# Performance work log

Measured on AMD Instinct MI355X. Metric: run time of the kernel, lower is better.

Reference implementation:

```python
import jax, jax.numpy as jnp
import numpy as np

SHAPES = ((80, 80), (40, 40), (20, 20), (10, 10))  # (H, W) per level
N_HEADS = 8
N_POINTS = 4
D_MODEL = 512  # double_d_model = 2*256 (densefusion=True)
D_FFN = 1024
B = 2
L = len(SHAPES)
S = sum(h * w for h, w in SHAPES)  # 8500
EPS = 1e-5


def _layernorm(x, g, b):
    m = jnp.mean(x, axis=-1, keepdims=True)
    v = jnp.mean((x - m) ** 2, axis=-1, keepdims=True)
    return (x - m) * jax.lax.rsqrt(v + EPS) * g + b


def _reference_points(shapes):
    # encoder get_reference_points with valid_ratios == 1 -> [S, 2] (x, y) in (0,1)
    refs = []
    for (H, W) in shapes:
        ry = (jnp.arange(H, dtype=jnp.float32) + 0.5) / H
        rx = (jnp.arange(W, dtype=jnp.float32) + 0.5) / W
        gy, gx = jnp.meshgrid(ry, rx, indexing='ij')
        refs.append(jnp.stack([gx.reshape(-1), gy.reshape(-1)], axis=-1))
    return jnp.concatenate(refs, axis=0)


def _sample_level(val, loc, H, W):
    # val: [B, H*W, h, d]; loc: [B, S, h, P, 2] normalized in [0,1]
    b, _, h, d = val.shape
    s, p = loc.shape[1], loc.shape[3]
    x = loc[..., 0] * W - 0.5
    y = loc[..., 1] * H - 0.5
    x0 = jnp.floor(x)
    y0 = jnp.floor(y)
    wx = x - x0
    wy = y - y0
    x0i = x0.astype(jnp.int32)
    y0i = y0.astype(jnp.int32)

    def gather(xi, yi):
        valid = ((xi >= 0) & (xi < W) & (yi >= 0) & (yi < H)).astype(val.dtype)
        idx = jnp.clip(yi, 0, H - 1) * W + jnp.clip(xi, 0, W - 1)  # [B,S,h,P]
        idx2 = jnp.transpose(idx, (0, 1, 3, 2)).reshape(b, s * p, h)  # [B,S*P,h]
        g = jnp.take_along_axis(val, idx2[..., None], axis=1)  # [B,S*P,h,d]
        vmask = jnp.transpose(valid, (0, 1, 3, 2))[..., None]  # [B,S,P,h,1]
        return g.reshape(b, s, p, h, d) * vmask

    v00 = gather(x0i, y0i)
    v01 = gather(x0i + 1, y0i)
    v10 = gather(x0i, y0i + 1)
    v11 = gather(x0i + 1, y0i + 1)
    wxT = jnp.transpose(wx, (0, 1, 3, 2))[..., None]
    wyT = jnp.transpose(wy, (0, 1, 3, 2))[..., None]
    return (v00 * (1 - wxT) * (1 - wyT) + v01 * wxT * (1 - wyT)
            + v10 * (1 - wxT) * wyT + v11 * wxT * wyT)  # [B,S,P,h,d]


def _forward(src, pos, w_off, b_off, w_attn, b_attn, w_val, b_val, w_out, b_out,
             ln1_g, ln1_b, w1, b1, w2, b2, ln2_g, ln2_b, shapes):
    b, s, c = src.shape
    h, p, l = N_HEADS, N_POINTS, len(shapes)
    d = c // h
    q = src + pos
    value = (src @ w_val + b_val).reshape(b, s, h, d)
    offsets = (q @ w_off + b_off).reshape(b, s, h, l, p, 2)
    attn = jax.nn.softmax((q @ w_attn + b_attn).reshape(b, s, h, l * p), axis=-1)
    attn = attn.reshape(b, s, h, l, p)
    ref = _reference_points(shapes)  # [S,2]
    # offset normalizer = (W_l, H_l)
    norm = jnp.array([[W, H] for (H, W) in shapes], dtype=src.dtype)  # [L,2]
    loc = ref[None, :, None, None, None, :] + offsets / norm[None, None, None, :, None, :]
    # split value per level and sample
    starts = np.cumsum([0] + [H * W for (H, W) in shapes])[:-1]
    sampled = []
    for lvl, (H, W) in enumerate(shapes):
        val_l = jax.lax.dynamic_slice_in_dim(value, int(starts[lvl]), H * W, axis=1)
        sampled.append(_sample_level(val_l, loc[:, :, :, lvl], H, W))
    sampled = jnp.stack(sampled)  # [L,B,S,P,h,d]
    out = jnp.einsum('lbqphd,bqhlp->bqhd', sampled, attn).reshape(b, s, c)
    attn_out = out @ w_out + b_out
    x = _layernorm(src + attn_out, ln1_g, ln1_b)
    ffn = jax.nn.relu(x @ w1 + b1) @ w2 + b2
    return _layernorm(x + ffn, ln2_g, ln2_b)


def setup_inputs() -> dict:
    key = jax.random.key(0)
    ks = jax.random.split(key, 20)
    sc = 0.02
    C = D_MODEL
    hLP = N_HEADS * L * N_POINTS
    f32 = jnp.float32
    inp = {
        'src': jax.random.normal(ks[0], (B, S, C), f32),
        'pos': jax.random.normal(ks[1], (B, S, C), f32),
        'w_off': jax.random.normal(ks[2], (C, hLP * 2), f32) * sc,
        'b_off': jax.random.normal(ks[3], (hLP * 2,), f32) * sc,
        'w_attn': jax.random.normal(ks[4], (C, hLP), f32) * sc,
        'b_attn': jax.random.normal(ks[5], (hLP,), f32) * sc,
        'w_val': jax.random.normal(ks[6], (C, C), f32) * sc,
        'b_val': jnp.zeros((C,), f32),
        'w_out': jax.random.normal(ks[7], (C, C), f32) * sc,
        'b_out': jnp.zeros((C,), f32),
        'ln1_g': jnp.ones((C,), f32),
        'ln1_b': jnp.zeros((C,), f32),
        'w1': jax.random.normal(ks[8], (C, D_FFN), f32) * sc,
        'b1': jnp.zeros((D_FFN,), f32),
        'w2': jax.random.normal(ks[9], (D_FFN, C), f32) * sc,
        'b2': jnp.zeros((C,), f32),
        'ln2_g': jnp.ones((C,), f32),
        'ln2_b': jnp.zeros((C,), f32),
        'spatial_shapes': jnp.array(SHAPES, dtype=jnp.int32),
    }
    return inp


def reference(src, pos, w_off, b_off, w_attn, b_attn, w_val, b_val, w_out, b_out,
              ln1_g, ln1_b, w1, b1, w2, b2, ln2_g, ln2_b, spatial_shapes):
    shapes = tuple((int(a), int(b)) for a, b in np.asarray(spatial_shapes))
    return _forward(src, pos, w_off, b_off, w_attn, b_attn, w_val, b_val, w_out, b_out,
                    ln1_g, ln1_b, w1, b1, w2, b2, ln2_g, ln2_b, shapes)
```

## Files before the change

### kernel.cpp

```cpp
#include <hip/hip_runtime.h>


typedef __bf16 bf16_t;
typedef __bf16 bf16x8 __attribute__((ext_vector_type(8)));
typedef __bf16 bf16x4 __attribute__((ext_vector_type(4)));
typedef float  f32x4  __attribute__((ext_vector_type(4)));
typedef float  f32x16 __attribute__((ext_vector_type(16)));

#define M_ROWS 17000
#define S_LEN  8500

__device__ inline void store_c(float* p, float v)  { *p = v; }
__device__ inline void store_c(bf16_t* p, float v) { *p = (bf16_t)v; }

__device__ inline float4 load4f(const float* p)  { return *(const float4*)p; }
__device__ inline float4 load4f(const bf16_t* p) {
    bf16x4 v = *(const bf16x4*)p;
    return make_float4((float)v[0], (float)v[1], (float)v[2], (float)v[3]);
}

__global__ __launch_bounds__(256)
void prep_kernel(const float* __restrict__ w_val, const float* __restrict__ w_off,
                 const float* __restrict__ w_attn, const float* __restrict__ w_out,
                 const float* __restrict__ w1, const float* __restrict__ w2,
                 const float* __restrict__ b_off, const float* __restrict__ b_attn,
                 bf16_t* __restrict__ wt_val, bf16_t* __restrict__ wt_oa,
                 bf16_t* __restrict__ wt_out, bf16_t* __restrict__ wt_w1,
                 bf16_t* __restrict__ wt_w2, float* __restrict__ bias_oa) {
    int z = blockIdx.z;
    if (z == 6) {
        if (blockIdx.x == 0 && blockIdx.y == 0) {
            for (int i = threadIdx.x; i < 384; i += 256)
                bias_oa[i] = (i < 256) ? b_off[i] : b_attn[i - 256];
        }
        return;
    }
    const float* in; bf16_t* out; int K, N;
    switch (z) {
        case 0: in = w_val;  out = wt_val;                     K = 512;  N = 512;  break;
        case 1: in = w_off;  out = wt_oa;                      K = 512;  N = 256;  break;
        case 2: in = w_attn; out = wt_oa + (size_t)256 * 512;  K = 512;  N = 128;  break;
        case 3: in = w_out;  out = wt_out;                     K = 512;  N = 512;  break;
        case 4: in = w1;     out = wt_w1;                      K = 512;  N = 1024; break;
        default: in = w2;    out = wt_w2;                      K = 1024; N = 512;  break;
    }
    int k0 = blockIdx.x * 32, n0 = blockIdx.y * 32;
    if (k0 >= K || n0 >= N) return;
    __shared__ float s[32][33];
    int tx = threadIdx.x & 31, ty = threadIdx.x >> 5;
    #pragma unroll
    for (int i = 0; i < 4; i++)
        s[ty + 8 * i][tx] = in[(size_t)(k0 + ty + 8 * i) * N + n0 + tx];
    __syncthreads();
    #pragma unroll
    for (int i = 0; i < 4; i++)
        out[(size_t)(n0 + ty + 8 * i) * K + k0 + tx] = (bf16_t)s[tx][ty + 8 * i];
}

__global__ __launch_bounds__(256)
void add_q_kernel(const float* __restrict__ a, const float* __restrict__ b,
                  bf16_t* __restrict__ q, bf16_t* __restrict__ src_bf, int n4) {
    int i = blockIdx.x * 256 + threadIdx.x;
    if (i >= n4) return;
    float4 av = *(const float4*)(a + (size_t)i * 4);
    float4 bv = *(const float4*)(b + (size_t)i * 4);
    bf16x4 sv, ov;
    sv[0] = (bf16_t)av.x; sv[1] = (bf16_t)av.y; sv[2] = (bf16_t)av.z; sv[3] = (bf16_t)av.w;
    ov[0] = (bf16_t)(av.x + bv.x);
    ov[1] = (bf16_t)(av.y + bv.y);
    ov[2] = (bf16_t)(av.z + bv.z);
    ov[3] = (bf16_t)(av.w + bv.w);
    *(bf16x4*)(q      + (size_t)i * 4) = ov;
    *(bf16x4*)(src_bf + (size_t)i * 4) = sv;
}

#define GEMM_CORE(A_PTR, WT_PTR, K_DIM, EPILOGUE)                                  \
    const int tid  = threadIdx.x;                                                  \
    const int wave = tid >> 6;                                                     \
    const int lane = tid & 63;                                                     \
    const int l31  = lane & 31;                                                    \
    const int lh8  = (lane >> 5) * 8;                                              \
    const int wr   = (wave >> 1) * 64;                                             \
    const int wc   = (wave & 1) * 64;                                              \
    const int row0 = blockIdx.x * 128;                                             \
    const int sr = tid >> 2;                                                       \
    const int sc = (tid & 3) * 8;                                                  \
    const bf16_t* gA0 = A_PTR  + (size_t)min(row0 + sr,      M_ROWS - 1) * K_DIM + sc; \
    const bf16_t* gA1 = A_PTR  + (size_t)min(row0 + sr + 64, M_ROWS - 1) * K_DIM + sc; \
    const bf16_t* gB0 = WT_PTR + (size_t)(col0 + sr) * K_DIM + sc;                 \
    const bf16_t* gB1 = WT_PTR + (size_t)(col0 + sr + 64) * K_DIM + sc;            \
    f32x16 acc[2][2];                                                              \
    _Pragma("unroll")                                                              \
    for (int i = 0; i < 2; i++)                                                    \
        _Pragma("unroll")                                                          \
        for (int j = 0; j < 2; j++)                                                \
            _Pragma("unroll")                                                      \
            for (int r = 0; r < 16; r++) acc[i][j][r] = 0.f;                       \
    bf16x8 pa0 = *(const bf16x8*)gA0;                                              \
    bf16x8 pa1 = *(const bf16x8*)gA1;                                              \
    bf16x8 pb0 = *(const bf16x8*)gB0;                                              \
    bf16x8 pb1 = *(const bf16x8*)gB1;                                              \
    const int nIter = K_DIM >> 5;                                                  \
    for (int it = 0; it < nIter; it++) {                                           \
        const int cur = it & 1;                                                    \
        *(bf16x8*)&As[cur][sr][sc]      = pa0;                                     \
        *(bf16x8*)&As[cur][sr + 64][sc] = pa1;                                     \
        *(bf16x8*)&Bs[cur][sr][sc]      = pb0;                                     \
        *(bf16x8*)&Bs[cur][sr + 64][sc] = pb1;                                     \
        __syncthreads();                                                           \
        if (it + 1 < nIter) {                                                      \
            int ko = (it + 1) << 5;                                                \
            pa0 = *(const bf16x8*)(gA0 + ko);                                      \
            pa1 = *(const bf16x8*)(gA1 + ko);                                      \
            pb0 = *(const bf16x8*)(gB0 + ko);                                      \
            pb1 = *(const bf16x8*)(gB1 + ko);                                      \
        }                                                                          \
        _Pragma("unroll")                                                          \
        for (int kh = 0; kh < 2; kh++) {                                           \
            bf16x8 a0 = *(const bf16x8*)&As[cur][wr + l31     ][kh * 16 + lh8];    \
            bf16x8 a1 = *(const bf16x8*)&As[cur][wr + 32 + l31][kh * 16 + lh8];    \
            bf16x8 b0 = *(const bf16x8*)&Bs[cur][wc + l31     ][kh * 16 + lh8];    \
            bf16x8 b1 = *(const bf16x8*)&Bs[cur][wc + 32 + l31][kh * 16 + lh8];    \
            acc[0][0] = __builtin_amdgcn_mfma_f32_32x32x16_bf16(a0, b0, acc[0][0], 0, 0, 0); \
            acc[0][1] = __builtin_amdgcn_mfma_f32_32x32x16_bf16(a0, b1, acc[0][1], 0, 0, 0); \
            acc[1][0] = __builtin_amdgcn_mfma_f32_32x32x16_bf16(a1, b0, acc[1][0], 0, 0, 0); \
            acc[1][1] = __builtin_amdgcn_mfma_f32_32x32x16_bf16(a1, b1, acc[1][1], 0, 0, 0); \
        }                                                                          \
    }                                                                              \
    EPILOGUE

template<typename OT, bool RELU>
__global__ __launch_bounds__(256)
void gemm128_kernel(const bf16_t* __restrict__ A, const bf16_t* __restrict__ Wt,
                    const float* __restrict__ bias, OT* __restrict__ Cout,
                    int N, int K) {
    __shared__ bf16_t As[2][128][40];
    __shared__ bf16_t Bs[2][128][40];
    const int col0 = blockIdx.y * 128;
    GEMM_CORE(A, Wt, K,
        {
            _Pragma("unroll")
            for (int i = 0; i < 2; i++)
                _Pragma("unroll")
                for (int j = 0; j < 2; j++) {
                    int col = col0 + wc + j * 32 + l31;
                    float bcol = bias[col];
                    _Pragma("unroll")
                    for (int reg = 0; reg < 16; reg++) {
                        int row = row0 + wr + i * 32 + (reg & 3) + 8 * (reg >> 2) + 4 * (lane >> 5);
                        if (row < M_ROWS) {
                            float v = acc[i][j][reg] + bcol;
                            if (RELU) v = fmaxf(v, 0.f);
                            store_c(Cout + (size_t)row * N + col, v);
                        }
                    }
                }
        }
    )
}

__global__ __launch_bounds__(256)
void gemm_voa_kernel(const bf16_t* __restrict__ src_bf, const bf16_t* __restrict__ q,
                     const bf16_t* __restrict__ wt_val, const bf16_t* __restrict__ wt_oa,
                     const float* __restrict__ b_val, const float* __restrict__ bias_oa,
                     bf16_t* __restrict__ value, float* __restrict__ oa) {
    __shared__ bf16_t As[2][128][40];
    __shared__ bf16_t Bs[2][128][40];
    const int by    = blockIdx.y;
    const bool isV  = by < 4;
    const int col0  = (isV ? by : by - 4) * 128;
    const bf16_t* Ap  = isV ? src_bf : q;
    const bf16_t* Wp  = isV ? wt_val : wt_oa;
    const float* bp   = isV ? b_val : bias_oa;
    const int Nout    = isV ? 512 : 384;
    GEMM_CORE(Ap, Wp, 512,
        {
            _Pragma("unroll")
            for (int i = 0; i < 2; i++)
                _Pragma("unroll")
                for (int j = 0; j < 2; j++) {
                    int col = col0 + wc + j * 32 + l31;
                    float bcol = bp[col];
                    _Pragma("unroll")
                    for (int reg = 0; reg < 16; reg++) {
                        int row = row0 + wr + i * 32 + (reg & 3) + 8 * (reg >> 2) + 4 * (lane >> 5);
                        if (row < M_ROWS) {
                            float v = acc[i][j][reg] + bcol;
                            if (isV) value[(size_t)row * 512 + col] = (bf16_t)v;
                            else     oa[(size_t)row * 384 + col] = v;
                        }
                    }
                }
        }
    )
}

__global__ __launch_bounds__(256)
void softmax16_kernel(float* __restrict__ oa, int ngroups) {
    int i = blockIdx.x * 256 + threadIdx.x;
    if (i >= ngroups) return;
    float* p = oa + (size_t)(i >> 3) * 384 + 256 + (i & 7) * 16;
    float v[16];
    float4* p4 = (float4*)p;
    #pragma unroll
    for (int j = 0; j < 4; j++) {
        float4 t = p4[j];
        v[4*j+0] = t.x; v[4*j+1] = t.y; v[4*j+2] = t.z; v[4*j+3] = t.w;
    }
    float mx = v[0];
    #pragma unroll
    for (int j = 1; j < 16; j++) mx = fmaxf(mx, v[j]);
    float sm = 0.f;
    #pragma unroll
    for (int j = 0; j < 16; j++) { v[j] = __expf(v[j] - mx); sm += v[j]; }
    float inv = 1.f / sm;
    #pragma unroll
    for (int j = 0; j < 4; j++)
        p4[j] = make_float4(v[4*j]*inv, v[4*j+1]*inv, v[4*j+2]*inv, v[4*j+3]*inv);
}

__global__ __launch_bounds__(256)
void sample_kernel(const bf16_t* __restrict__ value, const float* __restrict__ oa,
                   bf16_t* __restrict__ out) {
    int gw   = blockIdx.x * 4 + (threadIdx.x >> 6);
    int lane = threadIdx.x & 63;
    if (gw >= 2 * S_LEN * 8) return;
    int h  = gw & 7;
    int bs = gw >> 3;
    int b  = bs / S_LEN;
    int s  = bs - b * S_LEN;

    float rx, ry;
    if (s < 6400)      { int i = s;        float inv = 1.f/80.f; ry = ((i/80) + 0.5f)*inv; rx = ((i%80) + 0.5f)*inv; }
    else if (s < 8000) { int i = s - 6400; float inv = 1.f/40.f; ry = ((i/40) + 0.5f)*inv; rx = ((i%40) + 0.5f)*inv; }
    else if (s < 8400) { int i = s - 8000; float inv = 1.f/20.f; ry = ((i/20) + 0.5f)*inv; rx = ((i%20) + 0.5f)*inv; }
    else               { int i = s - 8400; float inv = 1.f/10.f; ry = ((i/10) + 0.5f)*inv; rx = ((i%10) + 0.5f)*inv; }

    const int WH[4]  = {80, 40, 20, 10};
    const int LST[4] = {0, 6400, 8000, 8400};

    int pt = lane >> 2;
    int cn = lane & 3;
    int ll = pt >> 2;
    int W  = WH[ll];
    const float* row = oa + (size_t)bs * 384;
    float2 o2 = *(const float2*)(row + h * 32 + pt * 2);
    float  aw = row[256 + h * 16 + pt];
    float x = fmaf(rx, (float)W, o2.x) - 0.5f;
    float y = fmaf(ry, (float)W, o2.y) - 0.5f;
    float fx = floorf(x), fy = floorf(y);
    float wx = x - fx,  wy = y - fy;
    int cx = (int)fx + (cn & 1);
    int cy = (int)fy + (cn >> 1);
    float wgt = aw * ((cn & 1) ? wx : 1.f - wx) * ((cn >> 1) ? wy : 1.f - wy);
    bool valid = (cx >= 0) && (cx < W) && (cy >= 0) && (cy < W);
    if (!valid) wgt = 0.f;
    int xc = min(max(cx, 0), W - 1);
    int yc = min(max(cy, 0), W - 1);
    int addr = LST[ll] + yc * W + xc;

    const bf16_t* vb = value + ((size_t)b * S_LEN) * 512 + h * 64 + (lane & 7) * 8;
    int sub = lane >> 3;
    float acc[8];
    #pragma unroll
    for (int j = 0; j < 8; j++) acc[j] = 0.f;
    #pragma unroll
    for (int it = 0; it < 8; it++) {
        int pair = it * 8 + sub;
        int   a = __shfl(addr, pair, 64);
        float w = __shfl(wgt,  pair, 64);
        bf16x8 v = *(const bf16x8*)(vb + (size_t)a * 512);
        #pragma unroll
        for (int j = 0; j < 8; j++) acc[j] += w * (float)v[j];
    }
    #pragma unroll
    for (int o = 8; o < 64; o <<= 1)
        #pragma unroll
        for (int j = 0; j < 8; j++) acc[j] += __shfl_xor(acc[j], o, 64);

    if (lane < 8) {
        bf16x8 ov;
        #pragma unroll
        for (int j = 0; j < 8; j++) ov[j] = (bf16_t)acc[j];
        *(bf16x8*)(out + (size_t)bs * 512 + h * 64 + lane * 8) = ov;
    }
}

template<typename INA, typename INB, typename OT>
__global__ __launch_bounds__(256)
void ln_kernel(const INA* __restrict__ Xa, const INB* __restrict__ Xb,
               const float* __restrict__ g, const float* __restrict__ be,
               OT* __restrict__ out, int M) {
    int wave = threadIdx.x >> 6;
    int lane = threadIdx.x & 63;
    int row = blockIdx.x * 4 + wave;
    if (row >= M) return;
    size_t base = (size_t)row * 512;
    float v[8];
    float s = 0.f, sq = 0.f;
    #pragma unroll
    for (int p = 0; p < 2; p++) {
        int idx = p * 256 + lane * 4;
        float4 a4 = load4f(Xa + base + idx);
        float4 b4 = load4f(Xb + base + idx);
        float t0 = a4.x + b4.x, t1 = a4.y + b4.y, t2 = a4.z + b4.z, t3 = a4.w + b4.w;
        v[p*4+0] = t0; v[p*4+1] = t1; v[p*4+2] = t2; v[p*4+3] = t3;
        s  += t0 + t1 + t2 + t3;
        sq += t0*t0 + t1*t1 + t2*t2 + t3*t3;
    }
    #pragma unroll
    for (int off = 32; off > 0; off >>= 1) {
        s  += __shfl_xor(s, off, 64);
        sq += __shfl_xor(sq, off, 64);
    }
    float mean = s * (1.f / 512.f);
    float var  = sq * (1.f / 512.f) - mean * mean;
    float rstd = rsqrtf(var + 1e-5f);
    #pragma unroll
    for (int p = 0; p < 2; p++) {
        int idx = p * 256 + lane * 4;
        #pragma unroll
        for (int j = 0; j < 4; j++) {
            int col = idx + j;
            float o = (v[p*4+j] - mean) * rstd * g[col] + be[col];
            store_c(out + base + col, o);
        }
    }
}

extern "C" void kernel_launch(void* const* d_in, const int* in_sizes, int n_in,
                              void* d_out, int out_size, void* d_ws, size_t ws_size,
                              hipStream_t stream) {
    const float* src    = (const float*)d_in[0];
    const float* pos    = (const float*)d_in[1];
    const float* w_off  = (const float*)d_in[2];
    const float* b_off  = (const float*)d_in[3];
    const float* w_attn = (const float*)d_in[4];
    const float* b_attn = (const float*)d_in[5];
    const float* w_val  = (const float*)d_in[6];
    const float* b_val  = (const float*)d_in[7];
    const float* w_out  = (const float*)d_in[8];
    const float* b_out  = (const float*)d_in[9];
    const float* ln1_g  = (const float*)d_in[10];
    const float* ln1_b  = (const float*)d_in[11];
    const float* w1     = (const float*)d_in[12];
    const float* b1     = (const float*)d_in[13];
    const float* w2     = (const float*)d_in[14];
    const float* b2     = (const float*)d_in[15];
    const float* ln2_g  = (const float*)d_in[16];
    const float* ln2_b  = (const float*)d_in[17];

    const int M = M_ROWS;
    char* ws = (char*)d_ws;
    size_t o = 0;
    auto alloc = [&](size_t bytes) { size_t r = o; o += (bytes + 255) & ~(size_t)255; return r; };

    size_t off_q       = alloc((size_t)M * 512 * 2);
    size_t off_srcbf   = alloc((size_t)M * 512 * 2);
    size_t off_value   = alloc((size_t)M * 512 * 2);
    size_t off_sampled = alloc((size_t)M * 512 * 2);
    size_t off_oa      = alloc((size_t)M * 384 * 4);
    size_t off_attnout = alloc((size_t)M * 512 * 2);
    size_t off_x       = alloc((size_t)M * 512 * 2);
    size_t off_wtval   = alloc((size_t)512 * 512 * 2);
    size_t off_wtoa    = alloc((size_t)384 * 512 * 2);
    size_t off_wtout   = alloc((size_t)512 * 512 * 2);
    size_t off_wtw1    = alloc((size_t)1024 * 512 * 2);
    size_t off_wtw2    = alloc((size_t)512 * 1024 * 2);
    size_t off_boa     = alloc((size_t)384 * 4);

    bf16_t* q        = (bf16_t*)(ws + off_q);
    bf16_t* src_bf   = (bf16_t*)(ws + off_srcbf);
    bf16_t* value    = (bf16_t*)(ws + off_value);
    bf16_t* sampled  = (bf16_t*)(ws + off_sampled);
    float*  oa       = (float*)(ws + off_oa);
    bf16_t* attn_out = (bf16_t*)(ws + off_attnout);
    bf16_t* x        = (bf16_t*)(ws + off_x);
    bf16_t* hidden   = (bf16_t*)(ws + off_sampled);
    bf16_t* ffn_out  = (bf16_t*)(ws + off_attnout);
    bf16_t* wt_val   = (bf16_t*)(ws + off_wtval);
    bf16_t* wt_oa    = (bf16_t*)(ws + off_wtoa);
    bf16_t* wt_out   = (bf16_t*)(ws + off_wtout);
    bf16_t* wt_w1    = (bf16_t*)(ws + off_wtw1);
    bf16_t* wt_w2    = (bf16_t*)(ws + off_wtw2);
    float*  bias_oa  = (float*)(ws + off_boa);
    float*  outp     = (float*)d_out;

    prep_kernel<<<dim3(32, 32, 7), 256, 0, stream>>>(
        w_val, w_off, w_attn, w_out, w1, w2, b_off, b_attn,
        wt_val, wt_oa, wt_out, wt_w1, wt_w2, bias_oa);

    add_q_kernel<<<(M * 512 / 4 + 255) / 256, 256, 0, stream>>>(src, pos, q, src_bf, M * 512 / 4);

    const int MT = (M + 127) / 128;

    gemm_voa_kernel<<<dim3(MT, 7), 256, 0, stream>>>(src_bf, q, wt_val, wt_oa, b_val, bias_oa, value, oa);

    softmax16_kernel<<<(M * 8 + 255) / 256, 256, 0, stream>>>(oa, M * 8);

    sample_kernel<<<(M * 8) / 4, 256, 0, stream>>>(value, oa, sampled);

    gemm128_kernel<bf16_t, false><<<dim3(MT, 4), 256, 0, stream>>>(sampled, wt_out, b_out, attn_out, 512, 512);

    ln_kernel<float, bf16_t, bf16_t><<<(M + 3) / 4, 256, 0, stream>>>(src, attn_out, ln1_g, ln1_b, x, M);

    gemm128_kernel<bf16_t, true ><<<dim3(MT, 8), 256, 0, stream>>>(x, wt_w1, b1, hidden, 1024, 512);
    gemm128_kernel<bf16_t, false><<<dim3(MT, 4), 256, 0, stream>>>(hidden, wt_w2, b2, ffn_out, 512, 1024);

    ln_kernel<bf16_t, bf16_t, float><<<(M + 3) / 4, 256, 0, stream>>>(x, ffn_out, ln2_g, ln2_b, outp, M);
}
```

Before: 389.7 us.

## Fuse attention softmax into sampling kernel and restructure per-query head mapping

```diff
diff --git a/kernel.cpp b/kernel.cpp
--- a/kernel.cpp
+++ b/kernel.cpp
@@ -4,6 +4,7 @@
 typedef __bf16 bf16_t;
 typedef __bf16 bf16x8 __attribute__((ext_vector_type(8)));
 typedef __bf16 bf16x4 __attribute__((ext_vector_type(4)));
+typedef float  f32x2  __attribute__((ext_vector_type(2)));
 typedef float  f32x4  __attribute__((ext_vector_type(4)));
 typedef float  f32x16 __attribute__((ext_vector_type(16)));
 
@@ -17,6 +18,10 @@
 __device__ inline float4 load4f(const bf16_t* p) {
     bf16x4 v = *(const bf16x4*)p;
     return make_float4((float)v[0], (float)v[1], (float)v[2], (float)v[3]);
+}
+
+__device__ inline void pk_fma(f32x2& a, f32x2 x, f32x2 y) {
+    asm("v_pk_fma_f32 %0, %1, %2, %0" : "+v"(a) : "v"(x), "v"(y));
 }
 
 __global__ __launch_bounds__(256)
@@ -172,7 +177,6 @@
     const bf16_t* Ap  = isV ? src_bf : q;
     const bf16_t* Wp  = isV ? wt_val : wt_oa;
     const float* bp   = isV ? b_val : bias_oa;
-    const int Nout    = isV ? 512 : 384;
     GEMM_CORE(Ap, Wp, 512,
         {
             _Pragma("unroll")
@@ -196,94 +200,109 @@
 }
 
 __global__ __launch_bounds__(256)
-void softmax16_kernel(float* __restrict__ oa, int ngroups) {
-    int i = blockIdx.x * 256 + threadIdx.x;
-    if (i >= ngroups) return;
-    float* p = oa + (size_t)(i >> 3) * 384 + 256 + (i & 7) * 16;
-    float v[16];
-    float4* p4 = (float4*)p;
-    #pragma unroll
-    for (int j = 0; j < 4; j++) {
-        float4 t = p4[j];
-        v[4*j+0] = t.x; v[4*j+1] = t.y; v[4*j+2] = t.z; v[4*j+3] = t.w;
-    }
-    float mx = v[0];
-    #pragma unroll
-    for (int j = 1; j < 16; j++) mx = fmaxf(mx, v[j]);
-    float sm = 0.f;
-    #pragma unroll
-    for (int j = 0; j < 16; j++) { v[j] = __expf(v[j] - mx); sm += v[j]; }
-    float inv = 1.f / sm;
-    #pragma unroll
-    for (int j = 0; j < 4; j++)
-        p4[j] = make_float4(v[4*j]*inv, v[4*j+1]*inv, v[4*j+2]*inv, v[4*j+3]*inv);
-}
-
-__global__ __launch_bounds__(256)
 void sample_kernel(const bf16_t* __restrict__ value, const float* __restrict__ oa,
                    bf16_t* __restrict__ out) {
-    int gw   = blockIdx.x * 4 + (threadIdx.x >> 6);
-    int lane = threadIdx.x & 63;
-    if (gw >= 2 * S_LEN * 8) return;
-    int h  = gw & 7;
-    int bs = gw >> 3;
-    int b  = bs / S_LEN;
-    int s  = bs - b * S_LEN;
+    __shared__ __align__(16) int sAW[4][2][8][68];
+    const int wave = threadIdx.x >> 6;
+    const int lane = threadIdx.x & 63;
+    const int h    = lane >> 3;
+    const int sub  = lane & 7;
+    const int bs   = blockIdx.x * 4 + wave;
+    const int b    = bs / S_LEN;
+    const int s    = bs - b * S_LEN;
 
     float rx, ry;
-    if (s < 6400)      { int i = s;        float inv = 1.f/80.f; ry = ((i/80) + 0.5f)*inv; rx = ((i%80) + 0.5f)*inv; }
-    else if (s < 8000) { int i = s - 6400; float inv = 1.f/40.f; ry = ((i/40) + 0.5f)*inv; rx = ((i%40) + 0.5f)*inv; }
-    else if (s < 8400) { int i = s - 8000; float inv = 1.f/20.f; ry = ((i/20) + 0.5f)*inv; rx = ((i%20) + 0.5f)*inv; }
-    else               { int i = s - 8400; float inv = 1.f/10.f; ry = ((i/10) + 0.5f)*inv; rx = ((i%10) + 0.5f)*inv; }
+    if (s < 6400)      { int i = s;        const float inv = 1.f/80.f; ry = ((i/80) + 0.5f)*inv; rx = ((i%80) + 0.5f)*inv; }
+    else if (s < 8000) { int i = s - 6400; const float inv = 1.f/40.f; ry = ((i/40) + 0.5f)*inv; rx = ((i%40) + 0.5f)*inv; }
+    else if (s < 8400) { int i = s - 8000; const float inv = 1.f/20.f; ry = ((i/20) + 0.5f)*inv; rx = ((i%20) + 0.5f)*inv; }
+    else               { int i = s - 8400; const float inv = 1.f/10.f; ry = ((i/10) + 0.5f)*inv; rx = ((i%10) + 0.5f)*inv; }
 
     const int WH[4]  = {80, 40, 20, 10};
     const int LST[4] = {0, 6400, 8000, 8400};
-
-    int pt = lane >> 2;
-    int cn = lane & 3;
-    int ll = pt >> 2;
-    int W  = WH[ll];
+    const int ll = sub >> 1;
+    const int W  = WH[ll];
+    const int LS = LST[ll];
+
     const float* row = oa + (size_t)bs * 384;
-    float2 o2 = *(const float2*)(row + h * 32 + pt * 2);
-    float  aw = row[256 + h * 16 + pt];
-    float x = fmaf(rx, (float)W, o2.x) - 0.5f;
-    float y = fmaf(ry, (float)W, o2.y) - 0.5f;
-    float fx = floorf(x), fy = floorf(y);
-    float wx = x - fx,  wy = y - fy;
-    int cx = (int)fx + (cn & 1);
-    int cy = (int)fy + (cn >> 1);
-    float wgt = aw * ((cn & 1) ? wx : 1.f - wx) * ((cn >> 1) ? wy : 1.f - wy);
-    bool valid = (cx >= 0) && (cx < W) && (cy >= 0) && (cy < W);
-    if (!valid) wgt = 0.f;
-    int xc = min(max(cx, 0), W - 1);
-    int yc = min(max(cy, 0), W - 1);
-    int addr = LST[ll] + yc * W + xc;
-
-    const bf16_t* vb = value + ((size_t)b * S_LEN) * 512 + h * 64 + (lane & 7) * 8;
-    int sub = lane >> 3;
-    float acc[8];
-    #pragma unroll
-    for (int j = 0; j < 8; j++) acc[j] = 0.f;
-    #pragma unroll
-    for (int it = 0; it < 8; it++) {
-        int pair = it * 8 + sub;
-        int   a = __shfl(addr, pair, 64);
-        float w = __shfl(wgt,  pair, 64);
-        bf16x8 v = *(const bf16x8*)(vb + (size_t)a * 512);
+    float4 o4 = *(const float4*)(row + h * 32 + sub * 4);
+    float2 lg = *(const float2*)(row + 256 + h * 16 + sub * 2);
+
+    float mx = fmaxf(lg.x, lg.y);
+    mx = fmaxf(mx, __shfl_xor(mx, 1, 64));
+    mx = fmaxf(mx, __shfl_xor(mx, 2, 64));
+    mx = fmaxf(mx, __shfl_xor(mx, 4, 64));
+    float e0 = __expf(lg.x - mx), e1 = __expf(lg.y - mx);
+    float sm = e0 + e1;
+    sm += __shfl_xor(sm, 1, 64);
+    sm += __shfl_xor(sm, 2, 64);
+    sm += __shfl_xor(sm, 4, 64);
+    float pinv = 1.f / sm;
+
+    #pragma unroll
+    for (int t = 0; t < 2; t++) {
+        float ox = t ? o4.z : o4.x;
+        float oy = t ? o4.w : o4.y;
+        float p  = (t ? e1 : e0) * pinv;
+        float x = fmaf(rx, (float)W, ox) - 0.5f;
+        float y = fmaf(ry, (float)W, oy) - 0.5f;
+        float fx = floorf(x), fy = floorf(y);
+        float wx = x - fx, wy = y - fy;
+        int ix = (int)fx, iy = (int)fy;
         #pragma unroll
-        for (int j = 0; j < 8; j++) acc[j] += w * (float)v[j];
-    }
-    #pragma unroll
-    for (int o = 8; o < 64; o <<= 1)
-        #pragma unroll
-        for (int j = 0; j < 8; j++) acc[j] += __shfl_xor(acc[j], o, 64);
-
-    if (lane < 8) {
-        bf16x8 ov;
-        #pragma unroll
-        for (int j = 0; j < 8; j++) ov[j] = (bf16_t)acc[j];
-        *(bf16x8*)(out + (size_t)bs * 512 + h * 64 + lane * 8) = ov;
-    }
+        for (int k2 = 0; k2 < 4; k2++) {
+            int cx = ix + (k2 & 1);
+            int cy = iy + (k2 >> 1);
+            float wgt = p * ((k2 & 1) ? wx : 1.f - wx) * ((k2 >> 1) ? wy : 1.f - wy);
+            if (cx < 0 || cx >= W || cy < 0 || cy >= W) wgt = 0.f;
+            int xc = min(max(cx, 0), W - 1);
+            int yc = min(max(cy, 0), W - 1);
+            int c = sub * 8 + t * 4 + k2;
+            sAW[wave][0][h][c] = LS + yc * W + xc;
+            sAW[wave][1][h][c] = __float_as_int(wgt);
+        }
+    }
+    __syncthreads();
+
+    const bf16_t* vb = value + ((size_t)b * S_LEN) * 512 + h * 64 + sub * 8;
+    f32x2 a01 = {0.f, 0.f}, a23 = {0.f, 0.f}, a45 = {0.f, 0.f}, a67 = {0.f, 0.f};
+
+    #define ACC8(V, WW) {                                                          \
+        f32x2 ws; ws[0] = (WW); ws[1] = (WW);                                      \
+        f32x2 pv;                                                                  \
+        pv[0] = __uint_as_float((V).x << 16);                                      \
+        pv[1] = __uint_as_float((V).x & 0xffff0000u); pk_fma(a01, pv, ws);         \
+        pv[0] = __uint_as_float((V).y << 16);                                      \
+        pv[1] = __uint_as_float((V).y & 0xffff0000u); pk_fma(a23, pv, ws);         \
+        pv[0] = __uint_as_float((V).z << 16);                                      \
+        pv[1] = __uint_as_float((V).z & 0xffff0000u); pk_fma(a45, pv, ws);         \
+        pv[0] = __uint_as_float((V).w << 16);                                      \
+        pv[1] = __uint_as_float((V).w & 0xffff0000u); pk_fma(a67, pv, ws); }
+
+    #pragma unroll 2
+    for (int c8 = 0; c8 < 64; c8 += 8) {
+        int4   ia = *(const int4*)  &sAW[wave][0][h][c8];
+        int4   ib = *(const int4*)  &sAW[wave][0][h][c8 + 4];
+        float4 wa = *(const float4*)&sAW[wave][1][h][c8];
+        float4 wb = *(const float4*)&sAW[wave][1][h][c8 + 4];
+        uint4 v0 = *(const uint4*)(vb + (size_t)ia.x * 512);
+        uint4 v1 = *(const uint4*)(vb + (size_t)ia.y * 512);
+        uint4 v2 = *(const uint4*)(vb + (size_t)ia.z * 512);
+        uint4 v3 = *(const uint4*)(vb + (size_t)ia.w * 512);
+        uint4 v4 = *(const uint4*)(vb + (size_t)ib.x * 512);
+        uint4 v5 = *(const uint4*)(vb + (size_t)ib.y * 512);
+        uint4 v6 = *(const uint4*)(vb + (size_t)ib.z * 512);
+        uint4 v7 = *(const uint4*)(vb + (size_t)ib.w * 512);
+        ACC8(v0, wa.x) ACC8(v1, wa.y) ACC8(v2, wa.z) ACC8(v3, wa.w)
+        ACC8(v4, wb.x) ACC8(v5, wb.y) ACC8(v6, wb.z) ACC8(v7, wb.w)
+    }
+    #undef ACC8
+
+    bf16x8 ov;
+    ov[0] = (bf16_t)a01[0]; ov[1] = (bf16_t)a01[1];
+    ov[2] = (bf16_t)a23[0]; ov[3] = (bf16_t)a23[1];
+    ov[4] = (bf16_t)a45[0]; ov[5] = (bf16_t)a45[1];
+    ov[6] = (bf16_t)a67[0]; ov[7] = (bf16_t)a67[1];
+    *(bf16x8*)(out + (size_t)bs * 512 + h * 64 + sub * 8) = ov;
 }
 
 template<typename INA, typename INB, typename OT>
@@ -396,9 +415,7 @@
 
     gemm_voa_kernel<<<dim3(MT, 7), 256, 0, stream>>>(src_bf, q, wt_val, wt_oa, b_val, bias_oa, value, oa);
 
-    softmax16_kernel<<<(M * 8 + 255) / 256, 256, 0, stream>>>(oa, M * 8);
-
-    sample_kernel<<<(M * 8) / 4, 256, 0, stream>>>(value, oa, sampled);
+    sample_kernel<<<M / 4, 256, 0, stream>>>(value, oa, sampled);
 
     gemm128_kernel<bf16_t, false><<<dim3(MT, 4), 256, 0, stream>>>(sampled, wt_out, b_out, attn_out, 512, 512);
 
```

After: 358.3 us. 1.09x faster.
